# Performance work log

Hardware: AMD Instinct MI355X
Metric: run time of the kernel (lower is better)

Reference implementation:

```python
import jax, jax.numpy as jnp
import numpy as np

B, H, W = 4, 64, 64
DIM, NH, HD = 768, 12, 64
MLP_DIM = 3072
WS = 14
EPS = 1e-6
SCALE = HD ** -0.5
QMIN, QMAX = -128.0, 127.0  # 8-bit signed fake-quant range


def fake_quant(x, s):
    # uniform quant-dequant with straight-through estimator
    q = jnp.clip(jnp.round(x / s), QMIN, QMAX) * s
    return x + jax.lax.stop_gradient(q - x)


def layer_norm(x, w, b):
    mu = jnp.mean(x, axis=-1, keepdims=True)
    var = jnp.var(x, axis=-1, keepdims=True)
    return (x - mu) * jax.lax.rsqrt(var + EPS) * w + b


def qlinear(x, w, b, a_s, w_s):
    # PreQuantizedLayer: fake-quant input activation and weight, then linear
    return fake_quant(x, a_s) @ fake_quant(w, w_s).T + b


def _attention(xw, qkv_w, qkv_b, proj_w, proj_b, rel_pos_h, rel_pos_w, a_s, w_s):
    Bw = xw.shape[0]
    N = WS * WS
    qkv = qlinear(xw.reshape(Bw, N, DIM), qkv_w, qkv_b, a_s[4], w_s[0])
    qkv = qkv.reshape(Bw, N, 3, NH, HD).transpose(2, 0, 3, 1, 4).reshape(3, Bw * NH, N, HD)
    q = fake_quant(qkv[0], a_s[0])
    k = fake_quant(qkv[1], a_s[1])
    v = fake_quant(qkv[2], a_s[2])
    attn = jnp.einsum('bqc,bkc->bqk', q * SCALE, k)  # (Bw*NH, N, N)
    # decomposed relative position bias (q_size == k_size == WS)
    idx = jnp.arange(WS)[:, None] - jnp.arange(WS)[None, :] + (WS - 1)
    Rh = rel_pos_h[idx]  # (WS, WS, HD)
    Rw = rel_pos_w[idx]
    r_q = q.reshape(Bw * NH, WS, WS, HD)
    rel_h = jnp.einsum('bhwc,hkc->bhwk', r_q, Rh)
    rel_w = jnp.einsum('bhwc,wkc->bhwk', r_q, Rw)
    attn = (attn.reshape(-1, WS, WS, WS, WS) + rel_h[..., :, None] + rel_w[..., None, :]).reshape(-1, N, N)
    attn = fake_quant(jax.nn.softmax(attn, axis=-1), a_s[3])
    out = jnp.einsum('bqk,bkc->bqc', attn, v)
    out = out.reshape(Bw, NH, WS, WS, HD).transpose(0, 2, 3, 1, 4).reshape(Bw, WS, WS, DIM)
    return qlinear(out, proj_w, proj_b, a_s[5], w_s[1])


def _forward(x, ln1_w, ln1_b, ln2_w, ln2_b, qkv_w, qkv_b, proj_w, proj_b,
             lin1_w, lin1_b, lin2_w, lin2_b, rel_pos_h, rel_pos_w, act_scales, w_scales):
    shortcut = x
    h = layer_norm(x, ln1_w, ln1_b)
    pad_h = (WS - H % WS) % WS
    pad_w = (WS - W % WS) % WS
    Hp, Wp = H + pad_h, W + pad_w
    hp = jnp.pad(h, ((0, 0), (0, pad_h), (0, pad_w), (0, 0)))
    win = hp.reshape(B, Hp // WS, WS, Wp // WS, WS, DIM).transpose(0, 1, 3, 2, 4, 5).reshape(-1, WS, WS, DIM)
    win = _attention(win, qkv_w, qkv_b, proj_w, proj_b, rel_pos_h, rel_pos_w, act_scales, w_scales)
    hp = win.reshape(B, Hp // WS, Wp // WS, WS, WS, DIM).transpose(0, 1, 3, 2, 4, 5).reshape(B, Hp, Wp, DIM)
    x = shortcut + hp[:, :H, :W, :]
    y = layer_norm(x, ln2_w, ln2_b)
    y = qlinear(y, lin1_w, lin1_b, act_scales[6], w_scales[2])
    y = jax.nn.gelu(y, approximate=False)
    y = qlinear(y, lin2_w, lin2_b, act_scales[7], w_scales[3])
    return x + y


def setup_inputs() -> dict:
    key = jax.random.key(0)
    ks = jax.random.split(key, 12)
    def w(k, shape, std=0.02):
        return jax.random.normal(k, shape, dtype=jnp.float32) * std
    return {
        'x': jax.random.normal(ks[0], (B, H, W, DIM), dtype=jnp.float32),
        'ln1_w': jnp.ones((DIM,), jnp.float32), 'ln1_b': jnp.zeros((DIM,), jnp.float32),
        'ln2_w': jnp.ones((DIM,), jnp.float32), 'ln2_b': jnp.zeros((DIM,), jnp.float32),
        'qkv_w': w(ks[1], (3 * DIM, DIM)), 'qkv_b': jnp.zeros((3 * DIM,), jnp.float32),
        'proj_w': w(ks[2], (DIM, DIM)), 'proj_b': jnp.zeros((DIM,), jnp.float32),
        'lin1_w': w(ks[3], (MLP_DIM, DIM)), 'lin1_b': jnp.zeros((MLP_DIM,), jnp.float32),
        'lin2_w': w(ks[4], (DIM, MLP_DIM)), 'lin2_b': jnp.zeros((DIM,), jnp.float32),
        'rel_pos_h': w(ks[5], (2 * WS - 1, HD)), 'rel_pos_w': w(ks[6], (2 * WS - 1, HD)),
        'act_scales': jax.random.uniform(ks[7], (8,), jnp.float32, 0.01, 0.06),
        'w_scales': jax.random.uniform(ks[8], (4,), jnp.float32, 0.0005, 0.003),
    }


def reference(x, ln1_w, ln1_b, ln2_w, ln2_b, qkv_w, qkv_b, proj_w, proj_b,
              lin1_w, lin1_b, lin2_w, lin2_b, rel_pos_h, rel_pos_w, act_scales, w_scales):
    return _forward(x, ln1_w, ln1_b, ln2_w, ln2_b, qkv_w, qkv_b, proj_w, proj_b,
                    lin1_w, lin1_b, lin2_w, lin2_b, rel_pos_h, rel_pos_w, act_scales, w_scales)
```

## Files before the change

kernel.cpp:

```cpp
#include <hip/hip_runtime.h>
#include <cstdint>


typedef int   v4i __attribute__((ext_vector_type(4)));
typedef float v4f __attribute__((ext_vector_type(4)));
typedef short v8s __attribute__((ext_vector_type(8)));
typedef int8_t i8;

__device__ __forceinline__ i8 satq(float x) {
  float q = rintf(x);
  q = fminf(127.f, fmaxf(-128.f, q));
  return (i8)(int)q;
}

__device__ __forceinline__ void gload16(const i8* g, i8* l) {
  __builtin_amdgcn_global_load_lds((const __attribute__((address_space(1))) void*)g,
                                   (__attribute__((address_space(3))) void*)l, 16, 0, 0);
}

__device__ __forceinline__ int pack4(const i8* q) {
  return ((int)(unsigned char)q[0]) | ((int)(unsigned char)q[1] << 8) |
         ((int)(unsigned char)q[2] << 16) | ((int)(unsigned char)q[3] << 24);
}

__device__ __forceinline__ float fast_gelu(float v) {
  float x = fabsf(v) * 0.70710678118654752f;
  float t = __builtin_amdgcn_rcpf(fmaf(0.3275911f, x, 1.0f));
  float s = fmaf(1.061405429f, t, -1.453152027f);
  s = fmaf(s, t, 1.421413741f);
  s = fmaf(s, t, -0.284496736f);
  s = fmaf(s, t, 0.254829592f);
  s = s * t;
  float e = __expf(-x * x);
  float erfa = fmaf(-s, e, 1.0f);
  float erfs = copysignf(erfa, v);
  float hv = 0.5f * v;
  return fmaf(hv, erfs, hv);
}

__global__ __launch_bounds__(256) void k_wquant(const float* __restrict__ w,
                                                i8* __restrict__ o, int n16,
                                                const float* __restrict__ wsc, int sidx) {
  int i = blockIdx.x * 256 + threadIdx.x;
  if (i >= n16) return;
  float inv = 1.0f / wsc[sidx];
  const float4* src = (const float4*)w + (size_t)i * 4;
  i8 buf[16];
#pragma unroll
  for (int t = 0; t < 4; t++) {
    float4 f = src[t];
    buf[t*4+0] = satq(f.x * inv); buf[t*4+1] = satq(f.y * inv);
    buf[t*4+2] = satq(f.z * inv); buf[t*4+3] = satq(f.w * inv);
  }
  *(v4i*)(o + (size_t)i * 16) = *(v4i*)buf;
}

__global__ __launch_bounds__(256) void k_relpack(const float* __restrict__ rph,
    const float* __restrict__ rpw, short* __restrict__ TB) {
  int g = blockIdx.x * 256 + threadIdx.x;
  if (g >= 1024) return;
  int lane = g & 63, c = g >> 6;
  int p = c & 1, ks = (c >> 1) & 1, nt = (c >> 2) & 1, tb = c >> 3;
  const float* src = tb ? rpw : rph;
  int n = nt * 16 + (lane & 15);
  int k0 = ks * 32 + (lane >> 4) * 8;
  short outv[8];
#pragma unroll
  for (int j = 0; j < 8; j++) {
    float v = (n < 27) ? src[n * 64 + k0 + j] : 0.f;
    unsigned u = __float_as_uint(v);
    unsigned hi = (u + 0x7fffu + ((u >> 16) & 1u)) >> 16;
    if (p == 0) outv[j] = (short)hi;
    else {
      float lof = v - __uint_as_float(hi << 16);
      unsigned ul = __float_as_uint(lof);
      outv[j] = (short)((ul + 0x7fffu + ((ul >> 16) & 1u)) >> 16);
    }
  }
  *(v8s*)(TB + (size_t)c * 512 + lane * 8) = *(v8s*)outv;
}

__global__ __launch_bounds__(256) void k_ln1(const float* __restrict__ x,
    const float* __restrict__ w, const float* __restrict__ b,
    const float* __restrict__ as, i8* __restrict__ outq) {
  int wt = blockIdx.x * 4 + (threadIdx.x >> 6);
  int lane = threadIdx.x & 63;
  int win = wt / 196, tok = wt - win * 196;
  int bb = win / 25, wrem = win - bb * 25, wh = wrem / 5, ww = wrem - wh * 5;
  int r = tok / 14, c = tok - r * 14;
  int y = wh * 14 + r, xx = ww * 14 + c;
  i8* dst = outq + (size_t)wt * 768 + lane * 12;
  if (y >= 64 || xx >= 64) {
    ((int*)dst)[0] = 0; ((int*)dst)[1] = 0; ((int*)dst)[2] = 0;
    return;
  }
  const float* row = x + (((size_t)bb * 64 + y) * 64 + xx) * 768 + lane * 12;
  float v[12];
  *(float4*)(v)     = *(const float4*)(row);
  *(float4*)(v + 4) = *(const float4*)(row + 4);
  *(float4*)(v + 8) = *(const float4*)(row + 8);
  float s = 0.f, ss = 0.f;
#pragma unroll
  for (int j = 0; j < 12; j++) { s += v[j]; ss += v[j] * v[j]; }
#pragma unroll
  for (int off = 1; off < 64; off <<= 1) { s += __shfl_xor(s, off); ss += __shfl_xor(ss, off); }
  float mu = s * (1.0f / 768.0f);
  float var = ss * (1.0f / 768.0f) - mu * mu;
  float rstd = 1.0f / sqrtf(var + 1e-6f);
  float inv = 1.0f / as[4];
  float wv[12], bv[12];
  *(float4*)(wv)     = *(const float4*)(w + lane * 12);
  *(float4*)(wv + 4) = *(const float4*)(w + lane * 12 + 4);
  *(float4*)(wv + 8) = *(const float4*)(w + lane * 12 + 8);
  *(float4*)(bv)     = *(const float4*)(b + lane * 12);
  *(float4*)(bv + 4) = *(const float4*)(b + lane * 12 + 4);
  *(float4*)(bv + 8) = *(const float4*)(b + lane * 12 + 8);
  i8 q[12];
#pragma unroll
  for (int j = 0; j < 12; j++) q[j] = satq(((v[j] - mu) * rstd * wv[j] + bv[j]) * inv);
  ((int*)dst)[0] = pack4(q); ((int*)dst)[1] = pack4(q + 4); ((int*)dst)[2] = pack4(q + 8);
}

__global__ __launch_bounds__(256) void k_ln2(const float* __restrict__ x2,
    const float* __restrict__ w, const float* __restrict__ b,
    const float* __restrict__ as, i8* __restrict__ outq) {
  int tokg = blockIdx.x * 4 + (threadIdx.x >> 6);
  int lane = threadIdx.x & 63;
  const float* row = x2 + (size_t)tokg * 768 + lane * 12;
  float v[12];
  *(float4*)(v)     = *(const float4*)(row);
  *(float4*)(v + 4) = *(const float4*)(row + 4);
  *(float4*)(v + 8) = *(const float4*)(row + 8);
  float s = 0.f, ss = 0.f;
#pragma unroll
  for (int j = 0; j < 12; j++) { s += v[j]; ss += v[j] * v[j]; }
#pragma unroll
  for (int off = 1; off < 64; off <<= 1) { s += __shfl_xor(s, off); ss += __shfl_xor(ss, off); }
  float mu = s * (1.0f / 768.0f);
  float var = ss * (1.0f / 768.0f) - mu * mu;
  float rstd = 1.0f / sqrtf(var + 1e-6f);
  float inv = 1.0f / as[6];
  float wv[12], bv[12];
  *(float4*)(wv)     = *(const float4*)(w + lane * 12);
  *(float4*)(wv + 4) = *(const float4*)(w + lane * 12 + 4);
  *(float4*)(wv + 8) = *(const float4*)(w + lane * 12 + 8);
  *(float4*)(bv)     = *(const float4*)(b + lane * 12);
  *(float4*)(bv + 4) = *(const float4*)(b + lane * 12 + 4);
  *(float4*)(bv + 8) = *(const float4*)(b + lane * 12 + 8);
  i8* dst = outq + (size_t)tokg * 768 + lane * 12;
  i8 q[12];
#pragma unroll
  for (int j = 0; j < 12; j++) q[j] = satq(((v[j] - mu) * rstd * wv[j] + bv[j]) * inv);
  ((int*)dst)[0] = pack4(q); ((int*)dst)[1] = pack4(q + 4); ((int*)dst)[2] = pack4(q + 8);
}

template <class Epi>
__global__ __launch_bounds__(256) void k_gemm(const i8* __restrict__ A, const i8* __restrict__ B,
                                              int M, int N, int K, Epi epi) {
  __shared__ __align__(16) i8 As[3][8192];
  __shared__ __align__(16) i8 Bs[3][8192];
  const int tid = threadIdx.x;
  const int lane = tid & 63, wave = tid >> 6;
  const int quad = lane >> 4, lc = lane & 15;
  const int wr = wave >> 1, wc = wave & 1;
  const long bm = (long)blockIdx.y * 128, bn = (long)blockIdx.x * 128;
  const v4i vz = {0, 0, 0, 0};
  v4i acc[4][4];
#pragma unroll
  for (int i = 0; i < 4; i++)
#pragma unroll
    for (int j = 0; j < 4; j++) acc[i][j] = vz;

  const int r0 = tid >> 2, c0 = tid & 3;
  const int cs = c0 ^ ((r0 >> 1) & 3);
  long rA0 = bm + r0;      if (rA0 >= M) rA0 = 0;
  long rA1 = bm + r0 + 64; if (rA1 >= M) rA1 = 0;
  const i8* pA0 = A + rA0 * (size_t)K + cs * 16;
  const i8* pA1 = A + rA1 * (size_t)K + cs * 16;
  const i8* pB0 = B + (bn + r0)      * (size_t)K + cs * 16;
  const i8* pB1 = B + (bn + r0 + 64) * (size_t)K + cs * 16;

  auto stage = [&](int buf) {
    gload16(pA0, As[buf] + tid * 16); gload16(pA1, As[buf] + 4096 + tid * 16);
    gload16(pB0, Bs[buf] + tid * 16); gload16(pB1, Bs[buf] + 4096 + tid * 16);
    pA0 += 64; pA1 += 64; pB0 += 64; pB1 += 64;
  };

  const int xq16 = (quad ^ ((lc >> 1) & 3)) * 16;

  auto compute = [&](int buf) {
    v4i af[4], bf[4];
#pragma unroll
    for (int i = 0; i < 4; i++) af[i] = *(const v4i*)(As[buf] + (wr * 64 + i * 16 + lc) * 64 + xq16);
#pragma unroll
    for (int j = 0; j < 4; j++) bf[j] = *(const v4i*)(Bs[buf] + (wc * 64 + j * 16 + lc) * 64 + xq16);
#pragma unroll
    for (int i = 0; i < 4; i++)
#pragma unroll
      for (int j = 0; j < 4; j++)
        acc[i][j] = __builtin_amdgcn_mfma_i32_16x16x64_i8(bf[j], af[i], acc[i][j], 0, 0, 0);
  };

  const int nt = K >> 6;
  stage(0); stage(1);
  int cb = 0, sb = 2;
  for (int t = 0; t < nt - 1; ++t) {
    asm volatile("s_waitcnt vmcnt(4)" ::: "memory");
    __builtin_amdgcn_s_barrier();
    asm volatile("" ::: "memory");
    if (t + 2 < nt) { stage(sb); if (++sb == 3) sb = 0; }
    compute(cb); if (++cb == 3) cb = 0;
  }
  asm volatile("s_waitcnt vmcnt(0)" ::: "memory");
  __builtin_amdgcn_s_barrier();
  asm volatile("" ::: "memory");
  compute(cb);

  Epi e = epi;
  e.init();
#pragma unroll
  for (int i = 0; i < 4; i++) {
    int gm = (int)bm + wr * 64 + i * 16 + lc;
#pragma unroll
    for (int j = 0; j < 4; j++) {
      int gn0 = (int)bn + wc * 64 + j * 16 + quad * 4;
      if (gm < M) e.store4(acc[i][j], gm, gn0);
    }
  }
}

struct EpiQKV {
  const float* as; const float* wsc; const float* bias;
  i8 *qq, *kq, *vt;
  float sab, invq, invk, invv;
  __device__ void init() {
    sab = as[4] * wsc[0]; invq = 1.f / as[0]; invk = 1.f / as[1]; invv = 1.f / as[2];
  }
  __device__ void store4(const v4i a, int m, int n0) {
    int t = n0 / 768, rem = n0 - t * 768;
    int head = rem >> 6, ch0 = rem & 63;
    int win = m / 196, tok = m - win * 196;
    size_t bh = (size_t)win * 12 + head;
    float4 bv = *(const float4*)(bias + n0);
    const float* bp = (const float*)&bv;
    if (t == 2) {
#pragma unroll
      for (int r = 0; r < 4; r++)
        vt[(bh * 64 + ch0 + r) * 256 + tok] = satq(((float)a[r] * sab + bp[r]) * invv);
    } else {
      float inv = (t == 0) ? invq : invk;
      i8 q[4];
#pragma unroll
      for (int r = 0; r < 4; r++) q[r] = satq(((float)a[r] * sab + bp[r]) * inv);
      *(int*)((t == 0 ? qq : kq) + (bh * 196 + tok) * 64 + ch0) = pack4(q);
    }
  }
};

struct EpiProj {
  const float* as; const float* wsc; const float* bias; const float* x0; float* out;
  float sab;
  __device__ void init() { sab = as[5] * wsc[1]; }
  __device__ void store4(const v4i a, int m, int n0) {
    int win = m / 196, tok = m - win * 196;
    int bb = win / 25, wrem = win - bb * 25, wh = wrem / 5, ww = wrem - wh * 5;
    int rr = tok / 14, cc = tok - rr * 14;
    int y = wh * 14 + rr, xx = ww * 14 + cc;
    if (y >= 64 || xx >= 64) return;
    size_t o = (((size_t)bb * 64 + y) * 64 + xx) * 768 + n0;
    float4 bv = *(const float4*)(bias + n0);
    float4 xv = *(const float4*)(x0 + o);
    float4 ov;
    ov.x = (float)a[0] * sab + bv.x + xv.x;
    ov.y = (float)a[1] * sab + bv.y + xv.y;
    ov.z = (float)a[2] * sab + bv.z + xv.z;
    ov.w = (float)a[3] * sab + bv.w + xv.w;
    *(float4*)(out + o) = ov;
  }
};

struct EpiLin1 {
  const float* as; const float* wsc; const float* bias; i8* outq;
  float sab, invg;
  __device__ void init() { sab = as[6] * wsc[2]; invg = 1.f / as[7]; }
  __device__ void store4(const v4i a, int m, int n0) {
    float4 bv = *(const float4*)(bias + n0);
    const float* bp = (const float*)&bv;
    i8 q[4];
#pragma unroll
    for (int r = 0; r < 4; r++) {
      float v = fmaf((float)a[r], sab, bp[r]);
      q[r] = satq(fast_gelu(v) * invg);
    }
    *(int*)(outq + (size_t)m * 3072 + n0) = pack4(q);
  }
};

struct EpiLin2 {
  const float* as; const float* wsc; const float* bias; float* out;
  float sab;
  __device__ void init() { sab = as[7] * wsc[3]; }
  __device__ void store4(const v4i a, int m, int n0) {
    size_t o = (size_t)m * 768 + n0;
    float4 bv = *(const float4*)(bias + n0);
    float4 ov = *(const float4*)(out + o);
    ov.x += (float)a[0] * sab + bv.x;
    ov.y += (float)a[1] * sab + bv.y;
    ov.z += (float)a[2] * sab + bv.z;
    ov.w += (float)a[3] * sab + bv.w;
    *(float4*)(out + o) = ov;
  }
};

__global__ __launch_bounds__(64, 4) void k_attn(const i8* __restrict__ qq, const i8* __restrict__ kq,
    const i8* __restrict__ vt, const short* __restrict__ TB,
    const float* __restrict__ as, i8* __restrict__ outq) {
  __shared__ __align__(16) i8 Ps[16 * 272];
  __shared__ float relS[16][66];
  const int t = blockIdx.x, bh = blockIdx.y;
  const int win = bh / 12, head = bh - win * 12;
  const int lane = threadIdx.x;
  const int quad = lane >> 4, lc = lane & 15;
  const float s0 = as[0];
  const float ssc = s0 * as[1] * 0.125f;
  const float invs3 = 1.0f / as[3];
  const float oscale = as[2] * as[3] / as[5];

  for (int idx = lane; idx < 256; idx += 64)
    *(int*)(Ps + (idx >> 4) * 272 + 192 + (idx & 15) * 4) = 0;

  unsigned ckhp[4] = {0, 0, 0, 0}, ckwp[4] = {0, 0, 0, 0};
#pragma unroll
  for (int f = 0; f < 13; f++) {
    int col = f * 16 + lc; if (col > 195) col = 195;
    int kh = col / 14, kw = col - kh * 14;
    ckhp[f >> 2] |= (unsigned)kh << ((f & 3) * 8);
    ckwp[f >> 2] |= (unsigned)kw << ((f & 3) * 8);
  }

  const v8s* TBv = (const v8s*)TB;
  const v4i vz = {0, 0, 0, 0};

  {
    int arow = t * 16 + lc; if (arow > 195) arow = 195;
    const i8* qrow = qq + ((size_t)bh * 196 + arow) * 64;
    v8s af[2];
#pragma unroll
    for (int ks = 0; ks < 2; ks++) {
      const i8* p = qrow + ks * 32 + quad * 8;
#pragma unroll
      for (int j = 0; j < 8; j++)
        af[ks][j] = (short)(__float_as_uint((float)p[j]) >> 16);
    }
    v4f rh0 = {0,0,0,0}, rh1 = {0,0,0,0}, rw0 = {0,0,0,0}, rw1 = {0,0,0,0};
#pragma unroll
    for (int ks = 0; ks < 2; ks++)
#pragma unroll
      for (int p2 = 0; p2 < 2; p2++) {
        rh0 = __builtin_amdgcn_mfma_f32_16x16x32_bf16(af[ks], TBv[(0*4 + ks*2 + p2)*64 + lane], rh0, 0, 0, 0);
        rh1 = __builtin_amdgcn_mfma_f32_16x16x32_bf16(af[ks], TBv[(1*4 + ks*2 + p2)*64 + lane], rh1, 0, 0, 0);
        rw0 = __builtin_amdgcn_mfma_f32_16x16x32_bf16(af[ks], TBv[(2*4 + ks*2 + p2)*64 + lane], rw0, 0, 0, 0);
        rw1 = __builtin_amdgcn_mfma_f32_16x16x32_bf16(af[ks], TBv[(3*4 + ks*2 + p2)*64 + lane], rw1, 0, 0, 0);
      }
#pragma unroll
    for (int r = 0; r < 4; r++) {
      int rl = quad * 4 + r;
      relS[rl][lc]      = rh0[r] * s0;
      relS[rl][16 + lc] = rh1[r] * s0;
      relS[rl][32 + lc] = rw0[r] * s0;
      relS[rl][48 + lc] = rw1[r] * s0;
    }
  }

  v4i aq = *(const v4i*)(qq + ((size_t)bh * 196 + t * 16 + lc) * 64 + quad * 16);
  v4i sacc[13];
#pragma unroll
  for (int f = 0; f < 13; f++) {
    v4i bk = *(const v4i*)(kq + ((size_t)bh * 196 + f * 16 + lc) * 64 + quad * 16);
    sacc[f] = __builtin_amdgcn_mfma_i32_16x16x64_i8(aq, bk, vz, 0, 0, 0);
  }

#pragma unroll
  for (int r = 0; r < 4; r++) {
    int rl = quad * 4 + r;
    int row = t * 16 + rl;
    int qh = row / 14, qw = row - qh * 14;
    const float* rH = &relS[rl][13 + qh];
    const float* rW = &relS[rl][32 + 13 + qw];
    float L[13];
#pragma unroll
    for (int f = 0; f < 13; f++) {
      int kh = (int)((ckhp[f >> 2] >> ((f & 3) * 8)) & 0xffu);
      int kw = (int)((ckwp[f >> 2] >> ((f & 3) * 8)) & 0xffu);
      L[f] = ((f < 12) | (lc < 4)) ? fmaf((float)sacc[f][r], ssc, rH[-kh] + rW[-kw]) : -1e30f;
    }
    float mx = L[0];
#pragma unroll
    for (int f = 1; f < 13; f++) mx = fmaxf(mx, L[f]);
#pragma unroll
    for (int off = 1; off < 16; off <<= 1) mx = fmaxf(mx, __shfl_xor(mx, off));
    float sum = 0.f;
#pragma unroll
    for (int f = 0; f < 13; f++) { float e = __expf(L[f] - mx); L[f] = e; sum += e; }
#pragma unroll
    for (int off = 1; off < 16; off <<= 1) sum += __shfl_xor(sum, off);
    float cq = (1.0f / sum) * invs3;
#pragma unroll
    for (int f = 0; f < 13; f++)
      Ps[rl * 272 + f * 16 + lc] = satq(L[f] * cq);
  }

  v4i oacc[4];
#pragma unroll
  for (int nt = 0; nt < 4; nt++) oacc[nt] = vz;
#pragma unroll
  for (int kc = 0; kc < 4; kc++) {
    v4i ap = *(const v4i*)(Ps + lc * 272 + kc * 64 + quad * 16);
#pragma unroll
    for (int nt = 0; nt < 4; nt++) {
      v4i bv = *(const v4i*)(vt + ((size_t)bh * 64 + nt * 16 + lc) * 256 + kc * 64 + quad * 16);
      oacc[nt] = __builtin_amdgcn_mfma_i32_16x16x64_i8(ap, bv, oacc[nt], 0, 0, 0);
    }
  }
#pragma unroll
  for (int nt = 0; nt < 4; nt++) {
    int ch = nt * 16 + lc;
#pragma unroll
    for (int r = 0; r < 4; r++) {
      int row = t * 16 + quad * 4 + r;
      if (row < 196)
        outq[((size_t)win * 196 + row) * 768 + head * 64 + ch] = satq((float)oacc[nt][r] * oscale);
    }
  }
}

extern "C" void kernel_launch(void* const* d_in, const int* in_sizes, int n_in,
                              void* d_out, int out_size, void* d_ws, size_t ws_size,
                              hipStream_t stream) {
  const float* x     = (const float*)d_in[0];
  const float* ln1w  = (const float*)d_in[1];
  const float* ln1b  = (const float*)d_in[2];
  const float* ln2w  = (const float*)d_in[3];
  const float* ln2b  = (const float*)d_in[4];
  const float* qkvw  = (const float*)d_in[5];
  const float* qkvb  = (const float*)d_in[6];
  const float* projw = (const float*)d_in[7];
  const float* projb = (const float*)d_in[8];
  const float* lin1w = (const float*)d_in[9];
  const float* lin1b = (const float*)d_in[10];
  const float* lin2w = (const float*)d_in[11];
  const float* lin2b = (const float*)d_in[12];
  const float* rph   = (const float*)d_in[13];
  const float* rpw   = (const float*)d_in[14];
  const float* as    = (const float*)d_in[15];
  const float* wsc   = (const float*)d_in[16];
  float* out = (float*)d_out;

  char* ws = (char*)d_ws;
  i8* big    = (i8*)ws;
  i8* qq     = big;
  i8* kq     = big + 15052800;
  i8* vt     = big + 30105600;
  short* TB  = (short*)(big + 49766400);
  i8* mlpq   = big;
  i8* creg   = (i8*)(ws + 50331648);
  i8* winq   = creg;
  i8* attno  = creg;
  i8* yq     = creg;
  i8* wqb    = (i8*)(ws + 65384448);
  i8* qkvwq  = wqb;
  i8* projwq = wqb + 1769472;
  i8* lin1wq = projwq + 589824;
  i8* lin2wq = lin1wq + 2359296;

  k_wquant<<<(110592 + 255) / 256, 256, 0, stream>>>(qkvw,  qkvwq,  110592, wsc, 0);
  k_wquant<<<( 36864 + 255) / 256, 256, 0, stream>>>(projw, projwq,  36864, wsc, 1);
  k_wquant<<<(147456 + 255) / 256, 256, 0, stream>>>(lin1w, lin1wq, 147456, wsc, 2);
  k_wquant<<<(147456 + 255) / 256, 256, 0, stream>>>(lin2w, lin2wq, 147456, wsc, 3);
  k_relpack<<<4, 256, 0, stream>>>(rph, rpw, TB);

  k_ln1<<<4900, 256, 0, stream>>>(x, ln1w, ln1b, as, winq);

  { EpiQKV e{as, wsc, qkvb, qq, kq, vt};
    k_gemm<EpiQKV><<<dim3(18, 154), 256, 0, stream>>>(winq, qkvwq, 19600, 2304, 768, e); }

  k_attn<<<dim3(13, 1200), 64, 0, stream>>>(qq, kq, vt, TB, as, attno);

  { EpiProj e{as, wsc, projb, x, out};
    k_gemm<EpiProj><<<dim3(6, 154), 256, 0, stream>>>(attno, projwq, 19600, 768, 768, e); }

  k_ln2<<<4096, 256, 0, stream>>>(out, ln2w, ln2b, as, yq);

  { EpiLin1 e{as, wsc, lin1b, mlpq};
    k_gemm<EpiLin1><<<dim3(24, 128), 256, 0, stream>>>(yq, lin1wq, 16384, 3072, 768, e); }

  { EpiLin2 e{as, wsc, lin2b, out};
    k_gemm<EpiLin2><<<dim3(6, 128), 256, 0, stream>>>(mlpq, lin2wq, 16384, 768, 3072, e); }
}
```

Baseline: 477.8 us.

## Rewrite int8 GEMM with 256x256 tiles, 8 waves, double-buffered phased pipeline and XCD remap

The int8 MFMA GEMM goes from 128x128 tiles with 4 waves and a triple-buffered K=64 pipeline to 256x256 tiles with 8 waves, K=128 stages and a 2-buffer ping-pong. Each stage is split into four barrier-separated phases with s_setprio around the MFMA bursts, and the next stage's global-to-LDS loads are issued in the first phase. Block indices are remapped from a 1D grid so consecutive tiles land on the same XCD for better L2 reuse. This aims for more data reuse per LDS byte and better overlap of loads with compute. In exchange it uses 128KB of LDS and 128 accumulator registers per thread, and the larger tiles leave fewer blocks and worse tail quantization on the smaller GEMMs.

```diff
diff --git a/kernel.cpp b/kernel.cpp
--- a/kernel.cpp
+++ b/kernel.cpp
@@ -154,80 +154,114 @@
   ((int*)dst)[0] = pack4(q); ((int*)dst)[1] = pack4(q + 4); ((int*)dst)[2] = pack4(q + 8);
 }
 
+#define PHASE(d, ih, jh, DOSTAGE, DOVM)                                        \
+  {                                                                            \
+    v4i af[4][2], bf[2][2];                                                    \
+    _Pragma("unroll") for (int i = 0; i < 4; i++)                              \
+      _Pragma("unroll") for (int kk = 0; kk < 2; kk++)                         \
+        af[i][kk] = *(const v4i*)(LA[d] +                                      \
+            (wm * 128 + ((ih) * 4 + i) * 16 + lc) * 128 +                      \
+            (((kk * 4 + quad) ^ xsw) * 16));                                   \
+    _Pragma("unroll") for (int j = 0; j < 2; j++)                              \
+      _Pragma("unroll") for (int kk = 0; kk < 2; kk++)                         \
+        bf[j][kk] = *(const v4i*)(LB[d] +                                      \
+            (wn * 64 + ((jh) * 2 + j) * 16 + lc) * 128 +                       \
+            (((kk * 4 + quad) ^ xsw) * 16));                                   \
+    if (DOSTAGE) {                                                             \
+      _Pragma("unroll") for (int s = 0; s < 4; s++) {                          \
+        gload16(pA[s], LA[(d) ^ 1] + s * 8192 + tid * 16); pA[s] += 128; }     \
+      _Pragma("unroll") for (int s = 0; s < 4; s++) {                          \
+        gload16(pB[s], LB[(d) ^ 1] + s * 8192 + tid * 16); pB[s] += 128; }     \
+    }                                                                          \
+    if (DOVM) { asm volatile("s_waitcnt vmcnt(0)" ::: "memory"); }             \
+    __builtin_amdgcn_sched_barrier(0);                                         \
+    __builtin_amdgcn_s_barrier();                                              \
+    asm volatile("s_waitcnt lgkmcnt(0)" ::: "memory");                         \
+    __builtin_amdgcn_sched_barrier(0);                                         \
+    __builtin_amdgcn_s_setprio(1);                                             \
+    _Pragma("unroll") for (int i = 0; i < 4; i++)                              \
+      _Pragma("unroll") for (int j = 0; j < 2; j++)                            \
+        _Pragma("unroll") for (int kk = 0; kk < 2; kk++)                       \
+          acc[(ih) * 4 + i][(jh) * 2 + j] =                                    \
+              __builtin_amdgcn_mfma_i32_16x16x64_i8(                           \
+                  bf[j][kk], af[i][kk], acc[(ih) * 4 + i][(jh) * 2 + j],       \
+                  0, 0, 0);                                                    \
+    __builtin_amdgcn_s_setprio(0);                                             \
+    __builtin_amdgcn_sched_barrier(0);                                         \
+    __builtin_amdgcn_s_barrier();                                              \
+  }
+
+#define GROUP(d, hn)          \
+  PHASE(d, 0, 0, (hn), false) \
+  PHASE(d, 0, 1, false, false)\
+  PHASE(d, 1, 0, false, false)\
+  PHASE(d, 1, 1, false, (hn))
+
 template <class Epi>
-__global__ __launch_bounds__(256) void k_gemm(const i8* __restrict__ A, const i8* __restrict__ B,
-                                              int M, int N, int K, Epi epi) {
-  __shared__ __align__(16) i8 As[3][8192];
-  __shared__ __align__(16) i8 Bs[3][8192];
+__global__ __launch_bounds__(512) void k_gemm(const i8* __restrict__ A, const i8* __restrict__ B,
+                                              int M, int N, int K, int nbx, Epi epi) {
+  __shared__ __align__(16) i8 LA[2][32768];
+  __shared__ __align__(16) i8 LB[2][32768];
   const int tid = threadIdx.x;
   const int lane = tid & 63, wave = tid >> 6;
   const int quad = lane >> 4, lc = lane & 15;
-  const int wr = wave >> 1, wc = wave & 1;
-  const long bm = (long)blockIdx.y * 128, bn = (long)blockIdx.x * 128;
+  const int xsw = lc >> 1;
+  const int wm = wave >> 2, wn = wave & 3;
+
+  const int nwg = gridDim.x;
+  const int orig = blockIdx.x;
+  const int qch = nwg >> 3, rch = nwg & 7;
+  const int xcd = orig & 7, idx = orig >> 3;
+  const int wg = (xcd < rch ? xcd * (qch + 1) : rch * (qch + 1) + (xcd - rch) * qch) + idx;
+  const int bx = wg % nbx, by = wg / nbx;
+  const long bm = (long)by * 256, bn = (long)bx * 256;
+
   const v4i vz = {0, 0, 0, 0};
-  v4i acc[4][4];
-#pragma unroll
-  for (int i = 0; i < 4; i++)
+  v4i acc[8][4];
+#pragma unroll
+  for (int i = 0; i < 8; i++)
 #pragma unroll
     for (int j = 0; j < 4; j++) acc[i][j] = vz;
 
-  const int r0 = tid >> 2, c0 = tid & 3;
-  const int cs = c0 ^ ((r0 >> 1) & 3);
-  long rA0 = bm + r0;      if (rA0 >= M) rA0 = 0;
-  long rA1 = bm + r0 + 64; if (rA1 >= M) rA1 = 0;
-  const i8* pA0 = A + rA0 * (size_t)K + cs * 16;
-  const i8* pA1 = A + rA1 * (size_t)K + cs * 16;
-  const i8* pB0 = B + (bn + r0)      * (size_t)K + cs * 16;
-  const i8* pB1 = B + (bn + r0 + 64) * (size_t)K + cs * 16;
-
-  auto stage = [&](int buf) {
-    gload16(pA0, As[buf] + tid * 16); gload16(pA1, As[buf] + 4096 + tid * 16);
-    gload16(pB0, Bs[buf] + tid * 16); gload16(pB1, Bs[buf] + 4096 + tid * 16);
-    pA0 += 64; pA1 += 64; pB0 += 64; pB1 += 64;
-  };
-
-  const int xq16 = (quad ^ ((lc >> 1) & 3)) * 16;
-
-  auto compute = [&](int buf) {
-    v4i af[4], bf[4];
-#pragma unroll
-    for (int i = 0; i < 4; i++) af[i] = *(const v4i*)(As[buf] + (wr * 64 + i * 16 + lc) * 64 + xq16);
-#pragma unroll
-    for (int j = 0; j < 4; j++) bf[j] = *(const v4i*)(Bs[buf] + (wc * 64 + j * 16 + lc) * 64 + xq16);
-#pragma unroll
-    for (int i = 0; i < 4; i++)
-#pragma unroll
-      for (int j = 0; j < 4; j++)
-        acc[i][j] = __builtin_amdgcn_mfma_i32_16x16x64_i8(bf[j], af[i], acc[i][j], 0, 0, 0);
-  };
-
-  const int nt = K >> 6;
-  stage(0); stage(1);
-  int cb = 0, sb = 2;
-  for (int t = 0; t < nt - 1; ++t) {
-    asm volatile("s_waitcnt vmcnt(4)" ::: "memory");
-    __builtin_amdgcn_s_barrier();
-    asm volatile("" ::: "memory");
-    if (t + 2 < nt) { stage(sb); if (++sb == 3) sb = 0; }
-    compute(cb); if (++cb == 3) cb = 0;
-  }
+  const int rbase = tid >> 3, c0 = tid & 7;
+  const int cs = c0 ^ ((tid >> 4) & 7);
+  const i8* pA[4];
+  const i8* pB[4];
+#pragma unroll
+  for (int s = 0; s < 4; s++) {
+    long rA = bm + rbase + 64 * s; if (rA >= M) rA = 0;
+    pA[s] = A + rA * (size_t)K + cs * 16;
+    pB[s] = B + (bn + rbase + 64 * s) * (size_t)K + cs * 16;
+  }
+
+#pragma unroll
+  for (int s = 0; s < 4; s++) { gload16(pA[s], LA[0] + s * 8192 + tid * 16); pA[s] += 128; }
+#pragma unroll
+  for (int s = 0; s < 4; s++) { gload16(pB[s], LB[0] + s * 8192 + tid * 16); pB[s] += 128; }
   asm volatile("s_waitcnt vmcnt(0)" ::: "memory");
   __builtin_amdgcn_s_barrier();
-  asm volatile("" ::: "memory");
-  compute(cb);
+
+  const int NT = K >> 7;
+  for (int t = 0; t < NT; t += 2) {
+    GROUP(0, true)
+    bool hn = (t + 2 < NT);
+    GROUP(1, hn)
+  }
 
   Epi e = epi;
   e.init();
 #pragma unroll
-  for (int i = 0; i < 4; i++) {
-    int gm = (int)bm + wr * 64 + i * 16 + lc;
+  for (int i = 0; i < 8; i++) {
+    int gm = (int)bm + wm * 128 + i * 16 + lc;
 #pragma unroll
     for (int j = 0; j < 4; j++) {
-      int gn0 = (int)bn + wc * 64 + j * 16 + quad * 4;
+      int gn0 = (int)bn + wn * 64 + j * 16 + quad * 4;
       if (gm < M) e.store4(acc[i][j], gm, gn0);
     }
   }
 }
+#undef PHASE
+#undef GROUP
 
 struct EpiQKV {
   const float* as; const float* wsc; const float* bias;
@@ -482,18 +516,18 @@
   k_ln1<<<4900, 256, 0, stream>>>(x, ln1w, ln1b, as, winq);
 
   { EpiQKV e{as, wsc, qkvb, qq, kq, vt};
-    k_gemm<EpiQKV><<<dim3(18, 154), 256, 0, stream>>>(winq, qkvwq, 19600, 2304, 768, e); }
+    k_gemm<EpiQKV><<<693, 512, 0, stream>>>(winq, qkvwq, 19600, 2304, 768, 9, e); }
 
   k_attn<<<dim3(13, 1200), 64, 0, stream>>>(qq, kq, vt, TB, as, attno);
 
   { EpiProj e{as, wsc, projb, x, out};
-    k_gemm<EpiProj><<<dim3(6, 154), 256, 0, stream>>>(attno, projwq, 19600, 768, 768, e); }
+    k_gemm<EpiProj><<<231, 512, 0, stream>>>(attno, projwq, 19600, 768, 768, 3, e); }
 
   k_ln2<<<4096, 256, 0, stream>>>(out, ln2w, ln2b, as, yq);
 
   { EpiLin1 e{as, wsc, lin1b, mlpq};
-    k_gemm<EpiLin1><<<dim3(24, 128), 256, 0, stream>>>(yq, lin1wq, 16384, 3072, 768, e); }
+    k_gemm<EpiLin1><<<768, 512, 0, stream>>>(yq, lin1wq, 16384, 3072, 768, 12, e); }
 
   { EpiLin2 e{as, wsc, lin2b, out};
-    k_gemm<EpiLin2><<<dim3(6, 128), 256, 0, stream>>>(mlpq, lin2wq, 16384, 768, 3072, e); }
-}
+    k_gemm<EpiLin2><<<192, 512, 0, stream>>>(mlpq, lin2wq, 16384, 768, 3072, 3, e); }
+}
```

New measurement: 501.4 us. +5.0%, slower.

## Merge prep kernels and keep attention probabilities in registers via transposed MFMA

Applied to the files above, without the earlier changes.

The four weight-quantization launches and the rel-pos packing launch are merged into a single prep kernel, cutting launch overhead. In the attention kernel the QK^T MFMA operands are swapped so each lane holds one query row. Softmax max and sum then need only two cross-quad shuffles instead of a 16-lane reduction. The quantized probabilities are packed in registers and redistributed with xor shuffles into the PV MFMA A-operand layout, removing the shared-memory Ps buffer and its stores and loads. The cost is more register pressure (a 13x4 float array) and added shuffle instructions.

```diff
diff --git a/kernel.cpp b/kernel.cpp
--- a/kernel.cpp
+++ b/kernel.cpp
@@ -38,46 +38,51 @@
   return fmaf(hv, erfs, hv);
 }
 
-__global__ __launch_bounds__(256) void k_wquant(const float* __restrict__ w,
-                                                i8* __restrict__ o, int n16,
-                                                const float* __restrict__ wsc, int sidx) {
-  int i = blockIdx.x * 256 + threadIdx.x;
-  if (i >= n16) return;
-  float inv = 1.0f / wsc[sidx];
-  const float4* src = (const float4*)w + (size_t)i * 4;
-  i8 buf[16];
-#pragma unroll
-  for (int t = 0; t < 4; t++) {
-    float4 f = src[t];
-    buf[t*4+0] = satq(f.x * inv); buf[t*4+1] = satq(f.y * inv);
-    buf[t*4+2] = satq(f.z * inv); buf[t*4+3] = satq(f.w * inv);
-  }
-  *(v4i*)(o + (size_t)i * 16) = *(v4i*)buf;
-}
-
-__global__ __launch_bounds__(256) void k_relpack(const float* __restrict__ rph,
-    const float* __restrict__ rpw, short* __restrict__ TB) {
-  int g = blockIdx.x * 256 + threadIdx.x;
-  if (g >= 1024) return;
-  int lane = g & 63, c = g >> 6;
-  int p = c & 1, ks = (c >> 1) & 1, nt = (c >> 2) & 1, tb = c >> 3;
-  const float* src = tb ? rpw : rph;
-  int n = nt * 16 + (lane & 15);
-  int k0 = ks * 32 + (lane >> 4) * 8;
-  short outv[8];
-#pragma unroll
-  for (int j = 0; j < 8; j++) {
-    float v = (n < 27) ? src[n * 64 + k0 + j] : 0.f;
-    unsigned u = __float_as_uint(v);
-    unsigned hi = (u + 0x7fffu + ((u >> 16) & 1u)) >> 16;
-    if (p == 0) outv[j] = (short)hi;
-    else {
-      float lof = v - __uint_as_float(hi << 16);
-      unsigned ul = __float_as_uint(lof);
-      outv[j] = (short)((ul + 0x7fffu + ((ul >> 16) & 1u)) >> 16);
-    }
-  }
-  *(v8s*)(TB + (size_t)c * 512 + lane * 8) = *(v8s*)outv;
+__global__ __launch_bounds__(256) void k_prep(const float* __restrict__ qkvw,
+    const float* __restrict__ projw, const float* __restrict__ lin1w,
+    const float* __restrict__ lin2w, i8* __restrict__ wqb,
+    const float* __restrict__ rph, const float* __restrict__ rpw,
+    short* __restrict__ TB, const float* __restrict__ wsc) {
+  int b = blockIdx.x;
+  if (b < 1728) {
+    int i = b * 256 + threadIdx.x;
+    const float* w; int base, sidx;
+    if (i < 110592)      { w = qkvw;  base = 0;      sidx = 0; }
+    else if (i < 147456) { w = projw; base = 110592; sidx = 1; }
+    else if (i < 294912) { w = lin1w; base = 147456; sidx = 2; }
+    else                 { w = lin2w; base = 294912; sidx = 3; }
+    float inv = 1.0f / wsc[sidx];
+    const float4* src = (const float4*)w + (size_t)(i - base) * 4;
+    i8 buf[16];
+#pragma unroll
+    for (int t = 0; t < 4; t++) {
+      float4 f = src[t];
+      buf[t*4+0] = satq(f.x * inv); buf[t*4+1] = satq(f.y * inv);
+      buf[t*4+2] = satq(f.z * inv); buf[t*4+3] = satq(f.w * inv);
+    }
+    *(v4i*)(wqb + (size_t)i * 16) = *(v4i*)buf;
+  } else {
+    int g = (b - 1728) * 256 + threadIdx.x;
+    int lane = g & 63, c = g >> 6;
+    int p = c & 1, ks = (c >> 1) & 1, nt = (c >> 2) & 1, tb = c >> 3;
+    const float* src = tb ? rpw : rph;
+    int n = nt * 16 + (lane & 15);
+    int k0 = ks * 32 + (lane >> 4) * 8;
+    short outv[8];
+#pragma unroll
+    for (int j = 0; j < 8; j++) {
+      float v = (n < 27) ? src[n * 64 + k0 + j] : 0.f;
+      unsigned u = __float_as_uint(v);
+      unsigned hi = (u + 0x7fffu + ((u >> 16) & 1u)) >> 16;
+      if (p == 0) outv[j] = (short)hi;
+      else {
+        float lof = v - __uint_as_float(hi << 16);
+        unsigned ul = __float_as_uint(lof);
+        outv[j] = (short)((ul + 0x7fffu + ((ul >> 16) & 1u)) >> 16);
+      }
+    }
+    *(v8s*)(TB + (size_t)c * 512 + lane * 8) = *(v8s*)outv;
+  }
 }
 
 __global__ __launch_bounds__(256) void k_ln1(const float* __restrict__ x,
@@ -315,7 +320,6 @@
 __global__ __launch_bounds__(64, 4) void k_attn(const i8* __restrict__ qq, const i8* __restrict__ kq,
     const i8* __restrict__ vt, const short* __restrict__ TB,
     const float* __restrict__ as, i8* __restrict__ outq) {
-  __shared__ __align__(16) i8 Ps[16 * 272];
   __shared__ float relS[16][66];
   const int t = blockIdx.x, bh = blockIdx.y;
   const int win = bh / 12, head = bh - win * 12;
@@ -326,18 +330,6 @@
   const float invs3 = 1.0f / as[3];
   const float oscale = as[2] * as[3] / as[5];
 
-  for (int idx = lane; idx < 256; idx += 64)
-    *(int*)(Ps + (idx >> 4) * 272 + 192 + (idx & 15) * 4) = 0;
-
-  unsigned ckhp[4] = {0, 0, 0, 0}, ckwp[4] = {0, 0, 0, 0};
-#pragma unroll
-  for (int f = 0; f < 13; f++) {
-    int col = f * 16 + lc; if (col > 195) col = 195;
-    int kh = col / 14, kw = col - kh * 14;
-    ckhp[f >> 2] |= (unsigned)kh << ((f & 3) * 8);
-    ckwp[f >> 2] |= (unsigned)kw << ((f & 3) * 8);
-  }
-
   const v8s* TBv = (const v8s*)TB;
   const v4i vz = {0, 0, 0, 0};
 
@@ -377,45 +369,89 @@
 #pragma unroll
   for (int f = 0; f < 13; f++) {
     v4i bk = *(const v4i*)(kq + ((size_t)bh * 196 + f * 16 + lc) * 64 + quad * 16);
-    sacc[f] = __builtin_amdgcn_mfma_i32_16x16x64_i8(aq, bk, vz, 0, 0, 0);
-  }
-
-#pragma unroll
-  for (int r = 0; r < 4; r++) {
-    int rl = quad * 4 + r;
-    int row = t * 16 + rl;
-    int qh = row / 14, qw = row - qh * 14;
-    const float* rH = &relS[rl][13 + qh];
-    const float* rW = &relS[rl][32 + 13 + qw];
-    float L[13];
-#pragma unroll
-    for (int f = 0; f < 13; f++) {
-      int kh = (int)((ckhp[f >> 2] >> ((f & 3) * 8)) & 0xffu);
-      int kw = (int)((ckwp[f >> 2] >> ((f & 3) * 8)) & 0xffu);
-      L[f] = ((f < 12) | (lc < 4)) ? fmaf((float)sacc[f][r], ssc, rH[-kh] + rW[-kw]) : -1e30f;
-    }
-    float mx = L[0];
-#pragma unroll
-    for (int f = 1; f < 13; f++) mx = fmaxf(mx, L[f]);
-#pragma unroll
-    for (int off = 1; off < 16; off <<= 1) mx = fmaxf(mx, __shfl_xor(mx, off));
-    float sum = 0.f;
-#pragma unroll
-    for (int f = 0; f < 13; f++) { float e = __expf(L[f] - mx); L[f] = e; sum += e; }
-#pragma unroll
-    for (int off = 1; off < 16; off <<= 1) sum += __shfl_xor(sum, off);
-    float cq = (1.0f / sum) * invs3;
-#pragma unroll
-    for (int f = 0; f < 13; f++)
-      Ps[rl * 272 + f * 16 + lc] = satq(L[f] * cq);
-  }
+    sacc[f] = __builtin_amdgcn_mfma_i32_16x16x64_i8(bk, aq, vz, 0, 0, 0);
+  }
+
+  unsigned khw[13];
+#pragma unroll
+  for (int f = 0; f < 13; f++) {
+    unsigned w0 = 0, w1 = 0, w2 = 0, w3 = 0;
+#pragma unroll
+    for (int r = 0; r < 4; r++) {
+      int k0 = f*16 + 0*4 + r; if (k0 > 195) k0 = 195;
+      int k1 = f*16 + 1*4 + r; if (k1 > 195) k1 = 195;
+      int k2 = f*16 + 2*4 + r; if (k2 > 195) k2 = 195;
+      int k3 = f*16 + 3*4 + r; if (k3 > 195) k3 = 195;
+      w0 |= (unsigned)(((k0/14) << 4) | (k0 - (k0/14)*14)) << (r*8);
+      w1 |= (unsigned)(((k1/14) << 4) | (k1 - (k1/14)*14)) << (r*8);
+      w2 |= (unsigned)(((k2/14) << 4) | (k2 - (k2/14)*14)) << (r*8);
+      w3 |= (unsigned)(((k3/14) << 4) | (k3 - (k3/14)*14)) << (r*8);
+    }
+    khw[f] = quad == 0 ? w0 : quad == 1 ? w1 : quad == 2 ? w2 : w3;
+  }
+
+  int qrow = t * 16 + lc;
+  int qh = qrow / 14, qw = qrow - qh * 14;
+  const float* rH = &relS[lc][13 + qh];
+  const float* rW = &relS[lc][32 + 13 + qw];
+  float L[13][4];
+  float mx = -1e30f;
+#pragma unroll
+  for (int f = 0; f < 13; f++)
+#pragma unroll
+    for (int r = 0; r < 4; r++) {
+      int kh = (int)((khw[f] >> (r * 8 + 4)) & 0xfu);
+      int kw = (int)((khw[f] >> (r * 8)) & 0xfu);
+      float v = ((f < 12) | (quad == 0))
+                  ? fmaf((float)sacc[f][r], ssc, rH[-kh] + rW[-kw]) : -1e30f;
+      L[f][r] = v;
+      mx = fmaxf(mx, v);
+    }
+  mx = fmaxf(mx, __shfl_xor(mx, 16));
+  mx = fmaxf(mx, __shfl_xor(mx, 32));
+  float sum = 0.f;
+#pragma unroll
+  for (int f = 0; f < 13; f++)
+#pragma unroll
+    for (int r = 0; r < 4; r++) { float e = __expf(L[f][r] - mx); L[f][r] = e; sum += e; }
+  sum += __shfl_xor(sum, 16);
+  sum += __shfl_xor(sum, 32);
+  float cq = (1.0f / sum) * invs3;
+
+  unsigned W[16];
+#pragma unroll
+  for (int f = 0; f < 13; f++) {
+    i8 q4[4];
+#pragma unroll
+    for (int r = 0; r < 4; r++) q4[r] = satq(L[f][r] * cq);
+    W[f] = (unsigned)pack4(q4);
+  }
+  W[13] = 0; W[14] = 0; W[15] = 0;
 
   v4i oacc[4];
 #pragma unroll
   for (int nt = 0; nt < 4; nt++) oacc[nt] = vz;
+  const bool q0m = (quad & 1) == 0, q1m = (quad & 2) == 0;
 #pragma unroll
   for (int kc = 0; kc < 4; kc++) {
-    v4i ap = *(const v4i*)(Ps + lc * 272 + kc * 64 + quad * 16);
+    unsigned a0 = W[kc*4+0], a1 = W[kc*4+1], a2 = W[kc*4+2], a3 = W[kc*4+3];
+    unsigned s0_ = (unsigned)__shfl_xor((int)a1, 16);
+    unsigned s1_ = (unsigned)__shfl_xor((int)a0, 16);
+    unsigned s2_ = (unsigned)__shfl_xor((int)a3, 16);
+    unsigned s3_ = (unsigned)__shfl_xor((int)a2, 16);
+    unsigned x0 = q0m ? a0 : s0_;
+    unsigned x1 = q0m ? s1_ : a1;
+    unsigned x2 = q0m ? a2 : s2_;
+    unsigned x3 = q0m ? s3_ : a3;
+    unsigned u0 = (unsigned)__shfl_xor((int)x2, 32);
+    unsigned u1 = (unsigned)__shfl_xor((int)x3, 32);
+    unsigned u2 = (unsigned)__shfl_xor((int)x0, 32);
+    unsigned u3 = (unsigned)__shfl_xor((int)x1, 32);
+    v4i ap;
+    ap[0] = (int)(q1m ? x0 : u0);
+    ap[1] = (int)(q1m ? x1 : u1);
+    ap[2] = (int)(q1m ? u2 : x2);
+    ap[3] = (int)(q1m ? u3 : x3);
 #pragma unroll
     for (int nt = 0; nt < 4; nt++) {
       v4i bv = *(const v4i*)(vt + ((size_t)bh * 64 + nt * 16 + lc) * 256 + kc * 64 + quad * 16);
@@ -473,11 +509,7 @@
   i8* lin1wq = projwq + 589824;
   i8* lin2wq = lin1wq + 2359296;
 
-  k_wquant<<<(110592 + 255) / 256, 256, 0, stream>>>(qkvw,  qkvwq,  110592, wsc, 0);
-  k_wquant<<<( 36864 + 255) / 256, 256, 0, stream>>>(projw, projwq,  36864, wsc, 1);
-  k_wquant<<<(147456 + 255) / 256, 256, 0, stream>>>(lin1w, lin1wq, 147456, wsc, 2);
-  k_wquant<<<(147456 + 255) / 256, 256, 0, stream>>>(lin2w, lin2wq, 147456, wsc, 3);
-  k_relpack<<<4, 256, 0, stream>>>(rph, rpw, TB);
+  k_prep<<<1732, 256, 0, stream>>>(qkvw, projw, lin1w, lin2w, wqb, rph, rpw, TB, wsc);
 
   k_ln1<<<4900, 256, 0, stream>>>(x, ln1w, ln1b, as, winq);
 
```

After: 520.9 us. 9.0% more time.
